# Performance work log

Measured on AMD Instinct MI355X. Metric: run time of the kernel, lower is better.

## Reference

```python
import jax, jax.numpy as jnp
import numpy as np

B, D, C = 4, 49, 512          # batch, tokens, in_features
N = 27                        # main nodes
NSUB = 14                     # sub nodes
C2 = C // 2                   # cross-attn q/k dim
BN_EPS = 1e-5
SCALE = C2 ** -0.5
# sub_list = [0,1,2,4,7,8,11]; each main node feeds two sub-sc rows
SUB_IDX = np.repeat(np.array([0, 1, 2, 4, 7, 8, 11]), 2)  # length 14


def _bn(x, w, b, axes):
    # training-mode batch norm (biased variance), matching nn.BatchNorm* forward math
    m = x.mean(axis=axes, keepdims=True)
    v = x.var(axis=axes, keepdims=True)
    return (x - m) * jax.lax.rsqrt(v + BN_EPS) * w + b


def _l2n(v):
    return v / jnp.maximum(jnp.linalg.norm(v, axis=-1, keepdims=True), 1e-12)


def setup_inputs() -> dict:
    key = jax.random.key(0)
    ks = iter(jax.random.split(key, 40))
    sC = float(np.sqrt(2.0 / C))
    sC2 = float(np.sqrt(2.0 / C2))
    W = lambda k, shape, sc: jax.random.normal(k, shape, jnp.float32) * sc
    inp = {}
    inp['x'] = jax.random.normal(next(ks), (B, D, C), jnp.float32)
    # 27 per-node LinearBlocks (fc + BN1d + relu), stacked
    inp['nb_W'] = W(next(ks), (N, C, C), sC)
    inp['nb_b'] = jnp.zeros((N, C), jnp.float32)
    inp['nb_bnw'] = jnp.ones((N, C), jnp.float32)
    inp['nb_bnb'] = jnp.zeros((N, C), jnp.float32)
    # FAM / ARM cross-attention params (torch Linear: [out,in] + bias)
    inp['fam_qW'] = W(next(ks), (C2, C), sC2); inp['fam_qb'] = jnp.zeros((C2,), jnp.float32)
    inp['fam_kW'] = W(next(ks), (C2, C), sC2); inp['fam_kb'] = jnp.zeros((C2,), jnp.float32)
    inp['fam_vW'] = W(next(ks), (C, C), sC);   inp['fam_vb'] = jnp.zeros((C,), jnp.float32)
    inp['arm_qW'] = W(next(ks), (C2, C), sC2); inp['arm_qb'] = jnp.zeros((C2,), jnp.float32)
    inp['arm_kW'] = W(next(ks), (C2, C), sC2); inp['arm_kb'] = jnp.zeros((C2,), jnp.float32)
    inp['arm_vW'] = W(next(ks), (C, C), sC);   inp['arm_vb'] = jnp.zeros((C,), jnp.float32)
    inp['ep_W'] = W(next(ks), (C, C), sC)
    inp['ep_b'] = jnp.zeros((C,), jnp.float32)
    inp['gem_bnw'] = jnp.ones((N * N,), jnp.float32)
    inp['gem_bnb'] = jnp.zeros((N * N,), jnp.float32)
    # 2 GatedGNN layers, 5 bias-free linears each
    inp['gnn_uW'] = W(next(ks), (2, C, C), sC)
    inp['gnn_vW'] = W(next(ks), (2, C, C), sC)
    inp['gnn_aW'] = W(next(ks), (2, C, C), sC)
    inp['gnn_bW'] = W(next(ks), (2, C, C), sC)
    inp['gnn_eW'] = W(next(ks), (2, C, C), sC)
    inp['gnn_bnvw'] = jnp.ones((2, N), jnp.float32)
    inp['gnn_bnvb'] = jnp.zeros((2, N), jnp.float32)
    inp['gnn_bnew'] = jnp.ones((2, N * N), jnp.float32)
    inp['gnn_bneb'] = jnp.zeros((2, N * N), jnp.float32)
    # similarity-calculation anchors (xavier-ish)
    inp['main_sc'] = W(next(ks), (N, C), float(np.sqrt(2.0 / (N + C))))
    inp['sub_sc'] = W(next(ks), (NSUB, C), float(np.sqrt(2.0 / (NSUB + C))))
    return inp


def _forward(x, nb_W, nb_b, nb_bnw, nb_bnb,
             fam_qW, fam_qb, fam_kW, fam_kb, fam_vW, fam_vb,
             arm_qW, arm_qb, arm_kW, arm_kb, arm_vW, arm_vb,
             ep_W, ep_b, gem_bnw, gem_bnb,
             gnn_uW, gnn_vW, gnn_aW, gnn_bW, gnn_eW,
             gnn_bnvw, gnn_bnvb, gnn_bnew, gnn_bneb,
             main_sc, sub_sc):
    # --- per-main-node LinearBlock, vmapped over the N node layers ---
    def node_block(W, b, bw, bb):
        h = x @ W.T + b                                   # [B,D,C]
        return jax.nn.relu(_bn(h, bw, bb, (0, 1)))        # BN1d over (batch, tokens)
    f_u = jax.vmap(node_block, in_axes=0, out_axes=1)(nb_W, nb_b, nb_bnw, nb_bnb)  # [B,N,D,C]
    f_v = f_u.mean(axis=2)                                # GAP -> [B,N,C]

    # --- GraphEdgeModel: FAM cross-attention (node tokens attend to global tokens) ---
    q = jnp.einsum('bndc,hc->bndh', f_u, fam_qW) + fam_qb # [B,N,D,C2]
    k = x @ fam_kW.T + fam_kb                             # [B,D,C2] (global feature = x, broadcast over N)
    v = x @ fam_vW.T + fam_vb                             # [B,D,C]
    attn = jax.nn.softmax(jnp.einsum('bndh,beh->bnde', q, k) * SCALE, axis=-1)
    feat = jnp.einsum('bnde,bec->bndc', attn, v)          # [B,N,D,C]

    # --- ARM cross-attention over all node pairs: edge e=i*N+j, query=feat[j] (start), key/value=feat[i] (end) ---
    Q = jnp.einsum('bndc,hc->bndh', feat, arm_qW) + arm_qb
    K = jnp.einsum('bndc,hc->bndh', feat, arm_kW) + arm_kb
    V = jnp.einsum('bndc,hc->bndh', feat, arm_vW) + arm_vb  # [B,N,D,C]
    dots = jnp.einsum('bjdh,bieh->bijde', Q, K) * SCALE     # [B,N,N,D,D]
    a2 = jax.nn.softmax(dots, axis=-1)
    fe = jnp.einsum('bijde,biec->bijdc', a2, V).reshape(B, N * N, D, C)

    edge = _bn(fe @ ep_W.T + ep_b,
               gem_bnw.reshape(1, -1, 1, 1), gem_bnb.reshape(1, -1, 1, 1), (0, 2, 3))
    f_e = edge.mean(axis=2).reshape(B, N, N, C)           # GAP over tokens -> [B,N,N,C]

    # --- 2 GatedGNN layers; start/end indicator einsums realized as broadcasts ---
    for l in range(2):
        res = f_v
        vi = f_v @ gnn_aW[l].T                            # end node i contribution
        vj = f_v @ gnn_bW[l].T                            # start node j contribution
        el = f_e @ gnn_eW[l].T
        m = vi[:, :, None, :] + vj[:, None, :, :] + el    # [B,N,N,C]
        m = _bn(m, gnn_bnew[l].reshape(1, N, N, 1), gnn_bneb[l].reshape(1, N, N, 1), (0, 3))
        f_e = f_e + jax.nn.relu(m)
        e = jax.nn.softmax(jax.nn.sigmoid(f_e), axis=2)   # softmax over start nodes j
        uj = f_v @ gnn_vW[l].T
        ui = f_v @ gnn_uW[l].T
        agg = ui + jnp.einsum('bijc,bjc->bic', e, uj) / N # scatter back to end node i
        f_v = res + jax.nn.relu(_bn(agg, gnn_bnvw[l].reshape(1, N, 1), gnn_bnvb[l].reshape(1, N, 1), (0, 2)))

    # --- SC layer: cosine similarity against relu+normalized anchors ---
    fvn = _l2n(f_v)
    main_cl = jnp.einsum('bnc,nc->bn', fvn, _l2n(jax.nn.relu(main_sc)))   # [B,27]
    sub_cl = jnp.einsum('bkc,kc->bk', fvn[:, SUB_IDX], _l2n(jax.nn.relu(sub_sc)))  # [B,14]
    return jnp.concatenate([main_cl, sub_cl], axis=-1)    # [B,41]


def reference(x, nb_W, nb_b, nb_bnw, nb_bnb,
              fam_qW, fam_qb, fam_kW, fam_kb, fam_vW, fam_vb,
              arm_qW, arm_qb, arm_kW, arm_kb, arm_vW, arm_vb,
              ep_W, ep_b, gem_bnw, gem_bnb,
              gnn_uW, gnn_vW, gnn_aW, gnn_bW, gnn_eW,
              gnn_bnvw, gnn_bnvb, gnn_bnew, gnn_bneb,
              main_sc, sub_sc):
    return _forward(x, nb_W, nb_b, nb_bnw, nb_bnb,
                    fam_qW, fam_qb, fam_kW, fam_kb, fam_vW, fam_vb,
                    arm_qW, arm_qb, arm_kW, arm_kb, arm_vW, arm_vb,
                    ep_W, ep_b, gem_bnw, gem_bnb,
                    gnn_uW, gnn_vW, gnn_aW, gnn_bW, gnn_eW,
                    gnn_bnvw, gnn_bnvb, gnn_bnew, gnn_bneb,
                    main_sc, sub_sc)
```

## Files before the change

kernel.cpp:

```cpp
#include <hip/hip_runtime.h>
#include <hip/hip_bf16.h>
#include <math.h>


namespace {

constexpr float SCALE_ = 0.0625f;
constexpr float EPS_   = 1e-5f;

typedef __attribute__((ext_vector_type(8))) short bf16x8;
typedef __attribute__((ext_vector_type(4))) short s16x4;
typedef __attribute__((ext_vector_type(4))) float f32x4;

__device__ __forceinline__ short f2bf(float f) {
  unsigned u = __float_as_uint(f);
  u += 0x7fffu + ((u >> 16) & 1u);
  return (short)(u >> 16);
}
__device__ __forceinline__ float bf2f(short h) {
  return __uint_as_float(((unsigned)(unsigned short)h) << 16);
}
__device__ __forceinline__ void split2(float f, short& h, short& l) {
  h = f2bf(f);
  l = f2bf(f - bf2f(h));
}

template<int CONVB>
__device__ __forceinline__
void gemm_bf3_core(const short* __restrict__ Ah, const short* __restrict__ Al,
                   const short* __restrict__ Wh, const short* __restrict__ Wl,
                   const float* __restrict__ Wf,
                   const float* __restrict__ bias, float* __restrict__ C,
                   short* __restrict__ Ch, short* __restrict__ Cl,
                   int M, int N, int K)
{
  __shared__ short sA[2][64][40];
  __shared__ short sB[2][64][40];
  const int tid  = threadIdx.x;
  const int n0   = blockIdx.x * 64, m0 = blockIdx.y * 64;
  const int wave = tid >> 6, lane = tid & 63;
  const int wr = (wave >> 1) * 32, wc = (wave & 1) * 32;
  const int lr = lane & 15, lk = (lane >> 4) * 8;
  const int sr = tid >> 2, sk = (tid & 3) * 8;
  const int arow = m0 + sr;

  f32x4 acc[2][2] = {};

  for (int k0 = 0; k0 < K; k0 += 32) {
    bf16x8 ah = {}, al = {};
    if (arow < M) {
      ah = *(const bf16x8*)(Ah + (long)arow * K + k0 + sk);
      al = *(const bf16x8*)(Al + (long)arow * K + k0 + sk);
    }
    bf16x8 bh, bl;
    if (CONVB) {
      f32x4 w0 = *(const f32x4*)(Wf + (long)(n0 + sr) * K + k0 + sk);
      f32x4 w1 = *(const f32x4*)(Wf + (long)(n0 + sr) * K + k0 + sk + 4);
#pragma unroll
      for (int j = 0; j < 4; ++j) {
        short h, l;
        split2(w0[j], h, l); bh[j] = h;     bl[j] = l;
        split2(w1[j], h, l); bh[4 + j] = h; bl[4 + j] = l;
      }
    } else {
      bh = *(const bf16x8*)(Wh + (long)(n0 + sr) * K + k0 + sk);
      bl = *(const bf16x8*)(Wl + (long)(n0 + sr) * K + k0 + sk);
    }
    __syncthreads();
    *(bf16x8*)&sA[0][sr][sk] = ah;
    *(bf16x8*)&sA[1][sr][sk] = al;
    *(bf16x8*)&sB[0][sr][sk] = bh;
    *(bf16x8*)&sB[1][sr][sk] = bl;
    __syncthreads();

    bf16x8 a0h = *(const bf16x8*)&sA[0][wr + lr][lk];
    bf16x8 a1h = *(const bf16x8*)&sA[0][wr + 16 + lr][lk];
    bf16x8 a0l = *(const bf16x8*)&sA[1][wr + lr][lk];
    bf16x8 a1l = *(const bf16x8*)&sA[1][wr + 16 + lr][lk];
    bf16x8 b0h = *(const bf16x8*)&sB[0][wc + lr][lk];
    bf16x8 b1h = *(const bf16x8*)&sB[0][wc + 16 + lr][lk];
    bf16x8 b0l = *(const bf16x8*)&sB[1][wc + lr][lk];
    bf16x8 b1l = *(const bf16x8*)&sB[1][wc + 16 + lr][lk];

    acc[0][0] = __builtin_amdgcn_mfma_f32_16x16x32_bf16(a0h, b0h, acc[0][0], 0, 0, 0);
    acc[0][1] = __builtin_amdgcn_mfma_f32_16x16x32_bf16(a0h, b1h, acc[0][1], 0, 0, 0);
    acc[1][0] = __builtin_amdgcn_mfma_f32_16x16x32_bf16(a1h, b0h, acc[1][0], 0, 0, 0);
    acc[1][1] = __builtin_amdgcn_mfma_f32_16x16x32_bf16(a1h, b1h, acc[1][1], 0, 0, 0);
    acc[0][0] = __builtin_amdgcn_mfma_f32_16x16x32_bf16(a0h, b0l, acc[0][0], 0, 0, 0);
    acc[0][1] = __builtin_amdgcn_mfma_f32_16x16x32_bf16(a0h, b1l, acc[0][1], 0, 0, 0);
    acc[1][0] = __builtin_amdgcn_mfma_f32_16x16x32_bf16(a1h, b0l, acc[1][0], 0, 0, 0);
    acc[1][1] = __builtin_amdgcn_mfma_f32_16x16x32_bf16(a1h, b1l, acc[1][1], 0, 0, 0);
    acc[0][0] = __builtin_amdgcn_mfma_f32_16x16x32_bf16(a0l, b0h, acc[0][0], 0, 0, 0);
    acc[0][1] = __builtin_amdgcn_mfma_f32_16x16x32_bf16(a0l, b1h, acc[0][1], 0, 0, 0);
    acc[1][0] = __builtin_amdgcn_mfma_f32_16x16x32_bf16(a1l, b0h, acc[1][0], 0, 0, 0);
    acc[1][1] = __builtin_amdgcn_mfma_f32_16x16x32_bf16(a1l, b1h, acc[1][1], 0, 0, 0);
  }

  const int rbase = m0 + wr + (lane >> 4) * 4;
  const int cb = n0 + wc + lr;
#pragma unroll
  for (int fj = 0; fj < 2; ++fj) {
    int col = cb + fj * 16;
    float bz = bias ? bias[col] : 0.f;
#pragma unroll
    for (int fi = 0; fi < 2; ++fi) {
#pragma unroll
      for (int r = 0; r < 4; ++r) {
        int row = rbase + fi * 16 + r;
        if (row < M) {
          float v = acc[fi][fj][r] + bz;
          long o = (long)row * N + col;
          if (C) C[o] = v;
          if (Ch) { short h, l; split2(v, h, l); Ch[o] = h; Cl[o] = l; }
        }
      }
    }
  }
}

template<int CONVB>
__global__ __launch_bounds__(256)
void gemm_bf3_k(const short* Ah, const short* Al, const short* Wh, const short* Wl,
                const float* Wf, const float* bias, float* C, short* Ch, short* Cl,
                int M, int N, int K, long aBS, long wBS, long bBS, long cBS)
{
  long z = blockIdx.z;
  gemm_bf3_core<CONVB>(Ah + z * aBS, Al + z * aBS,
                       Wh ? Wh + z * wBS : nullptr, Wl ? Wl + z * wBS : nullptr,
                       Wf ? Wf + z * wBS : nullptr,
                       bias ? bias + z * bBS : nullptr,
                       C ? C + z * cBS : nullptr,
                       Ch ? Ch + z * cBS : nullptr, Cl ? Cl + z * cBS : nullptr,
                       M, N, K);
}

struct G4 { const short* wh[4]; const short* wl[4]; float* c[4]; };

__global__ __launch_bounds__(256)
void gemm4_bf3_k(const short* Ah, const short* Al, G4 g, int M, int N, int K)
{
  int z = blockIdx.z;
  gemm_bf3_core<0>(Ah, Al, g.wh[z], g.wl[z], nullptr, nullptr, g.c[z],
                   nullptr, nullptr, M, N, K);
}

__global__ __launch_bounds__(256)
void cvt1_k(const float* __restrict__ s, short* __restrict__ dh,
            short* __restrict__ dl, int n4)
{
  long i = (long)blockIdx.x * 256 + threadIdx.x;
  if (i >= n4) return;
  f32x4 v = *(const f32x4*)(s + i * 4);
  s16x4 h, l;
#pragma unroll
  for (int j = 0; j < 4; ++j) { short hh, ll; split2(v[j], hh, ll); h[j] = hh; l[j] = ll; }
  *(s16x4*)(dh + i * 4) = h;
  *(s16x4*)(dl + i * 4) = l;
}

struct P10 { const float* s[10]; };

__global__ __launch_bounds__(256)
void cvt_w_k(P10 p, short* __restrict__ dh, short* __restrict__ dl)
{
  static const int tens[26] = {0,1,2,3,4,4,5,5,5,5,6,6,6,6,7,7,7,7,8,8,8,8,9,9,9,9};
  static const int coff[26] = {0,0,0,0,0,1,0,1,2,3,0,1,2,3,0,1,2,3,0,1,2,3,0,1,2,3};
  int c = blockIdx.y;
  const float* src = p.s[tens[c]] + (long)coff[c] * 131072;
  long dbase = (long)c * 131072;
  long i = ((long)blockIdx.x * 256 + threadIdx.x) * 8;
  f32x4 v0 = *(const f32x4*)(src + i);
  f32x4 v1 = *(const f32x4*)(src + i + 4);
  s16x4 h0, l0, h1, l1;
#pragma unroll
  for (int j = 0; j < 4; ++j) {
    short hh, ll;
    split2(v0[j], hh, ll); h0[j] = hh; l0[j] = ll;
    split2(v1[j], hh, ll); h1[j] = hh; l1[j] = ll;
  }
  *(s16x4*)(dh + dbase + i) = h0;     *(s16x4*)(dh + dbase + i + 4) = h1;
  *(s16x4*)(dl + dbase + i) = l0;     *(s16x4*)(dl + dbase + i + 4) = l1;
}

__global__ __launch_bounds__(256)
void gemm_nn_k(const float* __restrict__ A, const float* __restrict__ W,
               float* __restrict__ C, int M, int N, int K)
{
  __shared__ float As[32][68];
  __shared__ float Ws[32][68];
  const int tid = threadIdx.x;
  const int n0 = blockIdx.x * 64, m0 = blockIdx.y * 64;
  const int tx = tid & 15, ty = tid >> 4;
  float acc[4][4] = {};
  for (int k0 = 0; k0 < K; k0 += 32) {
#pragma unroll
    for (int p = 0; p < 2; ++p) {
      int idx = tid + p * 256;
      int row = idx >> 3, kq = idx & 7;
      float4 v = make_float4(0.f, 0.f, 0.f, 0.f);
      if (m0 + row < M)
        v = *(const float4*)(A + (long)(m0 + row) * K + k0 + kq * 4);
      As[kq*4+0][row] = v.x; As[kq*4+1][row] = v.y;
      As[kq*4+2][row] = v.z; As[kq*4+3][row] = v.w;
    }
#pragma unroll
    for (int p = 0; p < 2; ++p) {
      int idx = tid + p * 256;
      int row = idx >> 4, nq = idx & 15;
      float4 v = *(const float4*)(W + (long)(k0 + row) * N + n0 + nq * 4);
      *(float4*)&Ws[row][nq*4] = v;
    }
    __syncthreads();
#pragma unroll
    for (int k = 0; k < 32; ++k) {
      float4 a4 = *(const float4*)&As[k][ty*4];
      float4 b4 = *(const float4*)&Ws[k][tx*4];
      float av[4] = {a4.x, a4.y, a4.z, a4.w};
      float bv[4] = {b4.x, b4.y, b4.z, b4.w};
#pragma unroll
      for (int i2 = 0; i2 < 4; ++i2)
#pragma unroll
        for (int j2 = 0; j2 < 4; ++j2)
          acc[i2][j2] = fmaf(av[i2], bv[j2], acc[i2][j2]);
    }
    __syncthreads();
  }
#pragma unroll
  for (int i2 = 0; i2 < 4; ++i2) {
    int m = m0 + ty*4 + i2;
    if (m < M)
      *(float4*)(C + (long)m * N + n0 + tx*4) =
        make_float4(acc[i2][0], acc[i2][1], acc[i2][2], acc[i2][3]);
  }
}

__global__ __launch_bounds__(256)
void nb_stats(const float* __restrict__ H, float* __restrict__ mean, float* __restrict__ rs)
{
  int n = blockIdx.x;
  int c = blockIdx.y * 256 + threadIdx.x;
  const float* p = H + (long)n * 196 * 512 + c;
  float s = 0.f, q = 0.f;
  for (int r = 0; r < 196; ++r) { float v = p[(long)r * 512]; s += v; q = fmaf(v, v, q); }
  float m = s * (1.f / 196.f);
  float var = q * (1.f / 196.f) - m * m;
  mean[n * 512 + c] = m;
  rs[n * 512 + c] = rsqrtf(var + EPS_);
}

__global__ __launch_bounds__(256)
void nb_apply(const float* __restrict__ H, const float* __restrict__ mean,
              const float* __restrict__ rs, const float* __restrict__ bw,
              const float* __restrict__ bb,
              short* __restrict__ fuh, short* __restrict__ ful,
              float* __restrict__ fv, short* __restrict__ fvh, short* __restrict__ fvl)
{
  int n = blockIdx.x, b = blockIdx.y;
  int t = threadIdx.x;
#pragma unroll
  for (int cq = 0; cq < 2; ++cq) {
    int c = cq * 256 + t;
    float m = mean[n*512+c], r = rs[n*512+c];
    float w = bw[n*512+c], bias = bb[n*512+c];
    const float* hp = H + ((long)(n*4+b)*49) * 512 + c;
    long fo0 = ((long)(n*4+b)*49) * 512 + c;
    float s = 0.f;
    for (int d = 0; d < 49; ++d) {
      float v = hp[(long)d*512];
      float o = fmaxf(fmaf((v - m) * r, w, bias), 0.f);
      short hh, ll; split2(o, hh, ll);
      fuh[fo0 + (long)d*512] = hh;
      ful[fo0 + (long)d*512] = ll;
      s += o;
    }
    float fvv = s * (1.f / 49.f);
    long fo = ((long)b*27+n)*512 + c;
    fv[fo] = fvv;
    short hh, ll; split2(fvv, hh, ll);
    fvh[fo] = hh; fvl[fo] = ll;
  }
}

__global__ __launch_bounds__(512)
void attn_fam(const float* __restrict__ Qg, const float* __restrict__ Kg,
              const float* __restrict__ Vg, short* __restrict__ feath,
              short* __restrict__ featl)
{
  __shared__ float Qs[52][68];
  __shared__ float Ks[52][68];
  __shared__ float Ss[49][56];
  __shared__ float Vs[49][68];

  const int tid = threadIdx.x;
  const int bx = blockIdx.x, b = blockIdx.y;
  const int qblk = bx*4 + b;
  const long obase = ((long)b*1323 + (long)bx*49) * 512;
  const float* qp = Qg + (long)qblk * (49 * 256);
  const float* kp = Kg + (long)b * (49 * 256);
  const float* vp = Vg + (long)b * (49 * 512);

  const int tx = tid & 15;
  const int ty4 = tid >> 4;

  float sacc[2][4] = {};
  const int d0 = ty4 * 2;
  const int e0 = tx * 4;
  const int eh0 = (e0+0)&7, eh1 = (e0+1)&7, eh2 = (e0+2)&7, eh3 = (e0+3)&7;
  const int er0 = (e0+0) > 51 ? 51 : (e0+0);
  const int er1 = (e0+1) > 51 ? 51 : (e0+1);
  const int er2 = (e0+2) > 51 ? 51 : (e0+2);
  const int er3 = (e0+3) > 51 ? 51 : (e0+3);
  for (int kc = 0; kc < 256; kc += 64) {
    for (int idx = tid; idx < 49 * 16; idx += 512) {
      int row = idx >> 4, kq = idx & 15;
      *(float4*)&Qs[row][kq*4] = *(const float4*)(qp + (long)row*256 + kc + kq*4);
      *(float4*)&Ks[row][(kq ^ (row & 7)) * 4] = *(const float4*)(kp + (long)row*256 + kc + kq*4);
    }
    __syncthreads();
    if (d0 < 49) {
      const float* q0 = &Qs[d0][0];
      const float* q1 = &Qs[d0 + 1][0];
      const float* k0 = &Ks[er0][0];
      const float* k1 = &Ks[er1][0];
      const float* k2 = &Ks[er2][0];
      const float* k3 = &Ks[er3][0];
#pragma unroll 4
      for (int kq = 0; kq < 16; ++kq) {
        float4 a0 = *(const float4*)(q0 + kq*4);
        float4 a1 = *(const float4*)(q1 + kq*4);
        float4 b0 = *(const float4*)(k0 + ((kq ^ eh0) * 4));
        float4 b1 = *(const float4*)(k1 + ((kq ^ eh1) * 4));
        float4 b2 = *(const float4*)(k2 + ((kq ^ eh2) * 4));
        float4 b3 = *(const float4*)(k3 + ((kq ^ eh3) * 4));
        float av0[4] = {a0.x, a0.y, a0.z, a0.w};
        float av1[4] = {a1.x, a1.y, a1.z, a1.w};
        float bv[4][4] = {{b0.x,b0.y,b0.z,b0.w},{b1.x,b1.y,b1.z,b1.w},
                          {b2.x,b2.y,b2.z,b2.w},{b3.x,b3.y,b3.z,b3.w}};
#pragma unroll
        for (int j2 = 0; j2 < 4; ++j2) {
#pragma unroll
          for (int qq = 0; qq < 4; ++qq) {
            sacc[0][j2] = fmaf(av0[qq], bv[j2][qq], sacc[0][j2]);
            sacc[1][j2] = fmaf(av1[qq], bv[j2][qq], sacc[1][j2]);
          }
        }
      }
    }
    __syncthreads();
  }
  if (d0 < 49) {
#pragma unroll
    for (int i2 = 0; i2 < 2; ++i2) {
      int d = d0 + i2;
      if (d < 49) {
#pragma unroll
        for (int j2 = 0; j2 < 4; ++j2) {
          int e = e0 + j2;
          if (e < 49) Ss[d][e] = sacc[i2][j2] * SCALE_;
        }
      }
    }
  }
  __syncthreads();

  if (tid < 49) {
    float mx = -1e30f;
    for (int e = 0; e < 49; ++e) mx = fmaxf(mx, Ss[tid][e]);
    float sum = 0.f;
    for (int e = 0; e < 49; ++e) { float ex = __expf(Ss[tid][e] - mx); Ss[tid][e] = ex; sum += ex; }
    float inv = 1.f / sum;
    for (int e = 0; e < 49; ++e) Ss[tid][e] *= inv;
  }
  __syncthreads();

  const int td = ty4;
  const bool has2 = (td + 32) < 49;
  for (int cc = 0; cc < 512; cc += 64) {
    for (int idx = tid; idx < 49 * 16; idx += 512) {
      int row = idx >> 4, cq = idx & 15;
      *(float4*)&Vs[row][cq*4] = *(const float4*)(vp + (long)row*512 + cc + cq*4);
    }
    __syncthreads();
    float pa[2][4] = {};
#pragma unroll 7
    for (int e = 0; e < 49; ++e) {
      float4 v4 = *(const float4*)&Vs[e][tx*4];
      float p0 = Ss[td][e];
      float p1 = has2 ? Ss[td + 32][e] : 0.f;
      pa[0][0] = fmaf(p0, v4.x, pa[0][0]); pa[0][1] = fmaf(p0, v4.y, pa[0][1]);
      pa[0][2] = fmaf(p0, v4.z, pa[0][2]); pa[0][3] = fmaf(p0, v4.w, pa[0][3]);
      pa[1][0] = fmaf(p1, v4.x, pa[1][0]); pa[1][1] = fmaf(p1, v4.y, pa[1][1]);
      pa[1][2] = fmaf(p1, v4.z, pa[1][2]); pa[1][3] = fmaf(p1, v4.w, pa[1][3]);
    }
    __syncthreads();
    s16x4 hh, ll;
#pragma unroll
    for (int j = 0; j < 4; ++j) { short h, l; split2(pa[0][j], h, l); hh[j] = h; ll[j] = l; }
    *(s16x4*)(feath + obase + (long)td*512 + cc + tx*4) = hh;
    *(s16x4*)(featl + obase + (long)td*512 + cc + tx*4) = ll;
    if (has2) {
#pragma unroll
      for (int j = 0; j < 4; ++j) { short h, l; split2(pa[1][j], h, l); hh[j] = h; ll[j] = l; }
      *(s16x4*)(feath + obase + (long)(td+32)*512 + cc + tx*4) = hh;
      *(s16x4*)(featl + obase + (long)(td+32)*512 + cc + tx*4) = ll;
    }
  }
}

__global__ __launch_bounds__(512)
void bias2red_k(const float* __restrict__ epW, const float* __restrict__ vb,
                const float* __restrict__ epb, float* __restrict__ bias2,
                float* __restrict__ b2st)
{
  int c = threadIdx.x;
  float s = epb[c];
  const float* r = epW + (long)c * 512;
  for (int k = 0; k < 512; ++k) s = fmaf(r[k], vb[k], s);
  bias2[c] = s;
  __shared__ float red[16];
  float s1 = s, s2 = s * s;
#pragma unroll
  for (int off = 32; off; off >>= 1) { s1 += __shfl_down(s1, off); s2 += __shfl_down(s2, off); }
  int lane = c & 63, wid = c >> 6;
  if (lane == 0) { red[wid] = s1; red[8 + wid] = s2; }
  __syncthreads();
  if (c == 0) {
    float a = 0.f, qq = 0.f;
#pragma unroll
    for (int w = 0; w < 8; ++w) { a += red[w]; qq += red[8 + w]; }
    b2st[0] = a; b2st[1] = qq;
  }
}

__constant__ unsigned char TI_c[28] = {0,1,1,2,2,2,3,3,3,3,4,4,4,4,4,5,5,5,5,5,5,6,6,6,6,6,6,6};
__constant__ unsigned char TJ_c[28] = {0,0,1,0,1,2,0,1,2,3,0,1,2,3,4,0,1,2,3,4,5,0,1,2,3,4,5,6};

__global__ __launch_bounds__(256)
void gmat_k(const float* __restrict__ VW, const float* __restrict__ b2,
            float* __restrict__ G, float* __restrict__ V1, float* __restrict__ Vb2)
{
  __shared__ float Vs[49][260];
  const int i = blockIdx.x, b = blockIdx.y;
  const int tid = threadIdx.x;
  const int wave = tid >> 6, lane = tid & 63;
  const int di = lane >> 3, ej = lane & 7;
  const float* vp = VW + ((long)b*1323 + (long)i*49) * 512;
  float gacc[7];
#pragma unroll
  for (int t = 0; t < 7; ++t) gacc[t] = 0.f;
  float s1 = 0.f, s2 = 0.f;

  for (int half = 0; half < 2; ++half) {
    __syncthreads();
    for (int idx = tid; idx < 49 * 64; idx += 256) {
      int r = idx >> 6, q = idx & 63;
      *(float4*)&Vs[r][q*4] = *(const float4*)(vp + (long)r*512 + half*256 + q*4);
    }
    __syncthreads();
    int tt = 0;
    for (int t = wave; t < 28; t += 4, ++tt) {
      int d = TI_c[t]*8 + di, e = TJ_c[t]*8 + ej;
      int dc = d > 48 ? 48 : d, ec = e > 48 ? 48 : e;
      float g = gacc[tt];
      for (int q = 0; q < 64; ++q) {
        float4 a = *(const float4*)&Vs[dc][q*4];
        float4 bq = *(const float4*)&Vs[ec][q*4];
        g = fmaf(a.x, bq.x, fmaf(a.y, bq.y, fmaf(a.z, bq.z, fmaf(a.w, bq.w, g))));
      }
      gacc[tt] = g;
    }
    if (tid < 49) {
      for (int c = 0; c < 256; ++c) {
        float v = Vs[tid][c];
        s1 += v; s2 = fmaf(v, b2[half*256 + c], s2);
      }
    }
  }
  long gbase = ((long)b*27 + i) * 2401;
  int tt = 0;
  for (int t = wave; t < 28; t += 4, ++tt) {
    int ti = TI_c[t], tj = TJ_c[t];
    int d = ti*8 + di, e = tj*8 + ej;
    if (d < 49 && e < 49) {
      G[gbase + d*49 + e] = gacc[tt];
      if (ti != tj) G[gbase + e*49 + d] = gacc[tt];
    }
  }
  if (tid < 49) {
    long o = ((long)b*27 + i) * 49 + tid;
    V1[o] = s1; Vb2[o] = s2;
  }
}

__global__ __launch_bounds__(64)
void arm_post(const float* __restrict__ S, const float* __restrict__ G,
              const float* __restrict__ V1, const float* __restrict__ Vb2,
              float* __restrict__ Pbar, float* __restrict__ parts)
{
  __shared__ float TP[49 * 53];
  __shared__ float TG[49 * 53];
  const int tid = threadIdx.x;
  const int x = blockIdx.x, b = blockIdx.y;
  const int i = x / 27, j = x - i * 27;
  const float* Sp = S + (long)b*1323*1344 + (long)j*49*1344 + (long)i*49;
  for (int idx = tid; idx < 2401; idx += 64) {
    unsigned d = ((unsigned)idx * 1338u) >> 16;
    unsigned e = (unsigned)idx - d * 49u;
    TP[d*53 + e] = Sp[(long)d*1344 + e];
  }
  const float* Gp = G + ((long)b*27 + i) * 2401;
  for (int idx = tid; idx < 2401; idx += 64) {
    unsigned d = ((unsigned)idx * 1338u) >> 16;
    unsigned e = (unsigned)idx - d * 49u;
    TG[d*53 + e] = Gp[idx];
  }
  __syncthreads();
  if (tid < 49) {
    float* pr = &TP[tid * 53];
    float mx = -1e30f;
    for (int e = 0; e < 49; ++e) mx = fmaxf(mx, pr[e]);
    float sum = 0.f;
    for (int e = 0; e < 49; ++e) { float ex = __expf(pr[e] - mx); pr[e] = ex; sum += ex; }
    float inv = 1.f / sum;
    for (int e = 0; e < 49; ++e) pr[e] *= inv;
  }
  __syncthreads();
  float lin = 0.f, pvb = 0.f;
  if (tid < 49) {
    float pb = 0.f;
    for (int d = 0; d < 49; ++d) pb += TP[d*53 + tid];
    Pbar[(((long)b*27 + i)*27 + j)*49 + tid] = pb;
    long vo = ((long)b*27 + i)*49 + tid;
    lin = pb * V1[vo];
    pvb = pb * Vb2[vo];
  }
  float q2 = 0.f;
  if (tid < 49) {
    const float* pr = &TP[tid * 53];
#pragma unroll 1
    for (int e = 0; e < 49; e += 7) {
      float t0=0.f,t1=0.f,t2=0.f,t3=0.f,t4=0.f,t5=0.f,t6=0.f;
      for (int e2 = 0; e2 < 49; ++e2) {
        float pv = pr[e2];
        const float* g = &TG[e2*53 + e];
        t0 = fmaf(pv, g[0], t0); t1 = fmaf(pv, g[1], t1);
        t2 = fmaf(pv, g[2], t2); t3 = fmaf(pv, g[3], t3);
        t4 = fmaf(pv, g[4], t4); t5 = fmaf(pv, g[5], t5);
        t6 = fmaf(pv, g[6], t6);
      }
      q2 += t0*pr[e] + t1*pr[e+1] + t2*pr[e+2] + t3*pr[e+3]
          + t4*pr[e+4] + t5*pr[e+5] + t6*pr[e+6];
    }
  }
  float r1 = lin, r2 = q2 + 2.f * pvb;
#pragma unroll
  for (int off = 32; off; off >>= 1) { r1 += __shfl_down(r1, off); r2 += __shfl_down(r2, off); }
  if (tid == 0) {
    long o = ((long)b*729 + x) * 2;
    parts[o] = r1; parts[o + 1] = r2;
  }
}

__global__ __launch_bounds__(256)
void edge_fin(const float* __restrict__ parts, const float* __restrict__ b2st,
              float* __restrict__ ems)
{
  int e = blockIdx.x * 256 + threadIdx.x;
  if (e < 729) {
    float B1 = b2st[0], nb2 = b2st[1];
    float s = 196.f * B1, q = 196.f * nb2;
#pragma unroll
    for (int b = 0; b < 4; ++b) {
      s += parts[((long)b * 729 + e) * 2 + 0];
      q += parts[((long)b * 729 + e) * 2 + 1];
    }
    const float inv = 1.f / 100352.f;
    float m = s * inv;
    float var = q * inv - m * m;
    ems[e*2]   = m;
    ems[e*2+1] = rsqrtf(var + EPS_);
  }
}

__global__ __launch_bounds__(256)
void fe_build(const float* __restrict__ Pbar, const float* __restrict__ VW,
              const float* __restrict__ b2, const float* __restrict__ ems,
              const float* __restrict__ gw, const float* __restrict__ gb,
              float* __restrict__ fe, short* __restrict__ feh, short* __restrict__ fel)
{
  __shared__ float Pb[27 * 49];
  const int i = blockIdx.x, b = blockIdx.y;
  const int tid = threadIdx.x;
  const float* pp = Pbar + ((long)b*27 + i) * 27 * 49;
  for (int idx = tid; idx < 1323; idx += 256) Pb[idx] = pp[idx];
  __syncthreads();
  const float* vp = VW + ((long)b*1323 + (long)i*49) * 512;
#pragma unroll 1
  for (int half = 0; half < 2; ++half) {
    int c = half * 256 + tid;
    float acc[27];
#pragma unroll
    for (int j = 0; j < 27; ++j) acc[j] = 0.f;
    for (int e = 0; e < 49; ++e) {
      float v = vp[(long)e*512 + c];
#pragma unroll
      for (int j = 0; j < 27; ++j) acc[j] = fmaf(Pb[j*49 + e], v, acc[j]);
    }
    float bz = b2[c];
#pragma unroll
    for (int j = 0; j < 27; ++j) {
      int ij = i*27 + j;
      float m = ems[ij*2], rs = ems[ij*2+1];
      float h = acc[j] * (1.f/49.f) + bz;
      float v = fmaf((h - m) * rs, gw[ij], gb[ij]);
      long o = ((long)b*729 + ij)*512 + c;
      fe[o] = v;
      short hh, ll; split2(v, hh, ll);
      feh[o] = hh; fel[o] = ll;
    }
  }
}

__global__ __launch_bounds__(256)
void gnn_edge_bn(const float* __restrict__ vi, const float* __restrict__ vj,
                 const float* __restrict__ el, const float* __restrict__ wv,
                 const float* __restrict__ bv, float* fe,
                 short* __restrict__ feh, short* __restrict__ fel)
{
  int ij = blockIdx.x; int i = ij / 27, j = ij - i * 27;
  int t = threadIdx.x;
  __shared__ float red[18];
  float mv[8]; float s = 0.f, q = 0.f;
#pragma unroll
  for (int p = 0; p < 8; ++p) {
    int idx = p * 256 + t; int b = idx >> 9, c = idx & 511;
    float v = vi[((long)b*27+i)*512 + c] + vj[((long)b*27+j)*512 + c]
            + el[((long)b*729+ij)*512 + c];
    mv[p] = v; s += v; q = fmaf(v, v, q);
  }
  int lane = t & 63, wid = t >> 6;
#pragma unroll
  for (int off = 32; off; off >>= 1) { s += __shfl_down(s, off); q += __shfl_down(q, off); }
  if (lane == 0) { red[wid] = s; red[4 + wid] = q; }
  __syncthreads();
  if (t == 0) {
    float S = red[0]+red[1]+red[2]+red[3], Q = red[4]+red[5]+red[6]+red[7];
    float m = S * (1.f / 2048.f);
    red[16] = m;
    red[17] = rsqrtf(Q * (1.f / 2048.f) - m * m + EPS_);
  }
  __syncthreads();
  float m = red[16], rs = red[17];
  float w = wv[ij], bb = bv[ij];
#pragma unroll
  for (int p = 0; p < 8; ++p) {
    int idx = p * 256 + t; int b = idx >> 9, c = idx & 511;
    long o = ((long)b*729+ij)*512 + c;
    float nv = fe[o] + fmaxf(fmaf((mv[p] - m) * rs, w, bb), 0.f);
    fe[o] = nv;
    short hh, ll; split2(nv, hh, ll);
    feh[o] = hh; fel[o] = ll;
  }
}

__global__ __launch_bounds__(256)
void gnn_agg(const float* __restrict__ fe, const float* __restrict__ ui,
             const float* __restrict__ uj, float* __restrict__ agg)
{
  int i = blockIdx.x, b = blockIdx.y;
  int t = threadIdx.x;
#pragma unroll
  for (int cq = 0; cq < 2; ++cq) {
    int c = cq * 256 + t;
    float sg[27];
    float mx = -1e30f;
#pragma unroll
    for (int j = 0; j < 27; ++j) {
      float x = fe[((long)b*729 + i*27 + j)*512 + c];
      float sgm = 1.f / (1.f + __expf(-x));
      sg[j] = sgm; mx = fmaxf(mx, sgm);
    }
    float sum = 0.f;
#pragma unroll
    for (int j = 0; j < 27; ++j) { float e2 = __expf(sg[j] - mx); sg[j] = e2; sum += e2; }
    float acc = 0.f;
#pragma unroll
    for (int j = 0; j < 27; ++j)
      acc = fmaf(sg[j], uj[((long)b*27+j)*512 + c], acc);
    agg[((long)b*27+i)*512 + c] = ui[((long)b*27+i)*512 + c] + acc / (sum * 27.f);
  }
}

__global__ __launch_bounds__(256)
void gnn_node_bn(const float* __restrict__ agg, const float* __restrict__ wv,
                 const float* __restrict__ bv, float* fv,
                 short* __restrict__ fvh, short* __restrict__ fvl)
{
  int i = blockIdx.x;
  int t = threadIdx.x;
  __shared__ float red[18];
  float mv[8]; float s = 0.f, q = 0.f;
#pragma unroll
  for (int p = 0; p < 8; ++p) {
    int idx = p * 256 + t; int b = idx >> 9, c = idx & 511;
    float v = agg[((long)b*27+i)*512 + c];
    mv[p] = v; s += v; q = fmaf(v, v, q);
  }
  int lane = t & 63, wid = t >> 6;
#pragma unroll
  for (int off = 32; off; off >>= 1) { s += __shfl_down(s, off); q += __shfl_down(q, off); }
  if (lane == 0) { red[wid] = s; red[4 + wid] = q; }
  __syncthreads();
  if (t == 0) {
    float S = red[0]+red[1]+red[2]+red[3], Q = red[4]+red[5]+red[6]+red[7];
    float m = S * (1.f / 2048.f);
    red[16] = m;
    red[17] = rsqrtf(Q * (1.f / 2048.f) - m * m + EPS_);
  }
  __syncthreads();
  float m = red[16], rs = red[17];
  float w = wv[i], bb = bv[i];
#pragma unroll
  for (int p = 0; p < 8; ++p) {
    int idx = p * 256 + t; int b = idx >> 9, c = idx & 511;
    long o = ((long)b*27+i)*512 + c;
    float nv = fv[o] + fmaxf(fmaf((mv[p] - m) * rs, w, bb), 0.f);
    fv[o] = nv;
    short hh, ll; split2(nv, hh, ll);
    fvh[o] = hh; fvl[o] = ll;
  }
}

__constant__ int SUB_IDX_c[14] = {0,0,1,1,2,2,4,4,7,7,8,8,11,11};

__global__ __launch_bounds__(64)
void sc_k(const float* __restrict__ fv, const float* __restrict__ mainsc,
          const float* __restrict__ subsc, float* __restrict__ out)
{
  int o = blockIdx.x, b = blockIdx.y;
  int lane = threadIdx.x;
  int r; const float* ap;
  if (o < 27) { r = o; ap = mainsc + (long)o * 512; }
  else        { int k = o - 27; r = SUB_IDX_c[k]; ap = subsc + (long)k * 512; }
  const float* fp = fv + ((long)b*27 + r) * 512;
  float sff = 0.f, saa = 0.f, sfa = 0.f;
  for (int c = lane; c < 512; c += 64) {
    float f = fp[c];
    float a = fmaxf(ap[c], 0.f);
    sff = fmaf(f, f, sff); saa = fmaf(a, a, saa); sfa = fmaf(f, a, sfa);
  }
#pragma unroll
  for (int off = 32; off; off >>= 1) {
    sff += __shfl_down(sff, off); saa += __shfl_down(saa, off); sfa += __shfl_down(sfa, off);
  }
  if (lane == 0)
    out[b * 41 + o] = sfa / (fmaxf(sqrtf(sff), 1e-12f) * fmaxf(sqrtf(saa), 1e-12f));
}

}

extern "C" void kernel_launch(void* const* d_in, const int* in_sizes, int n_in,
                              void* d_out, int out_size, void* d_ws, size_t ws_size,
                              hipStream_t stream)
{
  (void)in_sizes; (void)n_in; (void)out_size; (void)ws_size;
  const float* x       = (const float*)d_in[0];
  const float* nb_W    = (const float*)d_in[1];
  const float* nb_b    = (const float*)d_in[2];
  const float* nb_bnw  = (const float*)d_in[3];
  const float* nb_bnb  = (const float*)d_in[4];
  const float* fam_qW  = (const float*)d_in[5];
  const float* fam_qb  = (const float*)d_in[6];
  const float* fam_kW  = (const float*)d_in[7];
  const float* fam_kb  = (const float*)d_in[8];
  const float* fam_vW  = (const float*)d_in[9];
  const float* fam_vb  = (const float*)d_in[10];
  const float* arm_qW  = (const float*)d_in[11];
  const float* arm_qb  = (const float*)d_in[12];
  const float* arm_kW  = (const float*)d_in[13];
  const float* arm_kb  = (const float*)d_in[14];
  const float* arm_vW  = (const float*)d_in[15];
  const float* arm_vb  = (const float*)d_in[16];
  const float* ep_W    = (const float*)d_in[17];
  const float* ep_b    = (const float*)d_in[18];
  const float* gem_bnw = (const float*)d_in[19];
  const float* gem_bnb = (const float*)d_in[20];
  const float* gnn_uW  = (const float*)d_in[21];
  const float* gnn_vW  = (const float*)d_in[22];
  const float* gnn_aW  = (const float*)d_in[23];
  const float* gnn_bW  = (const float*)d_in[24];
  const float* gnn_eW  = (const float*)d_in[25];
  const float* gnn_bnvw = (const float*)d_in[26];
  const float* gnn_bnvb = (const float*)d_in[27];
  const float* gnn_bnew = (const float*)d_in[28];
  const float* gnn_bneb = (const float*)d_in[29];
  const float* main_sc  = (const float*)d_in[30];
  const float* sub_sc   = (const float*)d_in[31];
  float* out = (float*)d_out;

  char* wp = (char*)d_ws;
  auto carveF = [&](long n) -> float* { float* p = (float*)wp; wp += ((n + 15) & ~15L) * 4; return p; };
  auto carveS = [&](long n) -> short* { short* p = (short*)wp; wp += ((n + 15) & ~15L) * 2; return p; };

  float* Hnb   = carveF((long)27*196*512);
  float* S     = carveF((long)4*1323*1344);
  float* fe    = carveF((long)4*729*512);
  float* kf    = carveF(196*256);
  float* vf    = carveF(196*512);
  float* qfam  = carveF((long)5292*256);
  float* nbm   = carveF(27*512);
  float* nbr   = carveF(27*512);
  float* Mpre  = carveF(512*512);
  float* bias2 = carveF(512);
  float* b2st  = carveF(16);
  float* parts = carveF(4*729*2);
  float* ems   = carveF(1460);
  float* G     = carveF((long)108*2401);
  float* V1    = carveF(108*49);
  float* Vb2   = carveF(108*49);
  float* Pbar  = carveF((long)4*27*27*49);
  float* fv    = carveF(108*512);
  float* vi    = carveF(108*512);
  float* vj    = carveF(108*512);
  float* uj    = carveF(108*512);
  float* ui    = carveF(108*512);
  float* agg   = carveF(108*512);
  float* VW = Hnb;
  float* el = S;

  short* xh    = carveS(100352);
  short* xl    = carveS(100352);
  short* wph   = carveS((long)26*131072);
  short* wpl   = carveS((long)26*131072);
  short* Mpreh = carveS(262144);
  short* Mprel = carveS(262144);
  short* fuh   = carveS((long)5292*512);
  short* ful   = carveS((long)5292*512);
  short* Qah   = carveS((long)5292*256);
  short* Qal   = carveS((long)5292*256);
  short* Kah   = carveS((long)4*1344*256);
  short* Kal   = carveS((long)4*1344*256);
  short* fvh   = carveS(108*512);
  short* fvl   = carveS(108*512);
  short* feath = fuh;
  short* featl = ful;
  short* feh   = Qah;
  short* fel   = Qal;
  fel = Kah;

  short* famqWh = wph + 0L*131072;        short* famqWl = wpl + 0L*131072;
  short* famkWh = wph + 1L*131072;        short* famkWl = wpl + 1L*131072;
  short* armqWh = wph + 2L*131072;        short* armqWl = wpl + 2L*131072;
  short* armkWh = wph + 3L*131072;        short* armkWl = wpl + 3L*131072;
  short* famvWh = wph + 4L*131072;        short* famvWl = wpl + 4L*131072;
  short* uWh    = wph + 6L*131072;        short* uWl    = wpl + 6L*131072;
  short* vWh    = wph + 10L*131072;       short* vWl    = wpl + 10L*131072;
  short* aWh    = wph + 14L*131072;       short* aWl    = wpl + 14L*131072;
  short* bWh    = wph + 18L*131072;       short* bWl    = wpl + 18L*131072;
  short* eWh    = wph + 22L*131072;       short* eWl    = wpl + 22L*131072;

  cvt1_k<<<dim3(98), 256, 0, stream>>>(x, xh, xl, 25088);
  P10 p10;
  p10.s[0] = fam_qW; p10.s[1] = fam_kW; p10.s[2] = arm_qW; p10.s[3] = arm_kW;
  p10.s[4] = fam_vW; p10.s[5] = gnn_uW; p10.s[6] = gnn_vW; p10.s[7] = gnn_aW;
  p10.s[8] = gnn_bW; p10.s[9] = gnn_eW;
  cvt_w_k<<<dim3(64, 26), 256, 0, stream>>>(p10, wph, wpl);

  gemm_bf3_k<1><<<dim3(8,4,27), 256, 0, stream>>>(xh, xl, nullptr, nullptr, nb_W,
      nb_b, Hnb, nullptr, nullptr, 196, 512, 512, 0, 262144, 512, 100352);
  nb_stats<<<dim3(27,2), 256, 0, stream>>>(Hnb, nbm, nbr);
  nb_apply<<<dim3(27,4), 256, 0, stream>>>(Hnb, nbm, nbr, nb_bnw, nb_bnb,
      fuh, ful, fv, fvh, fvl);
  gemm_bf3_k<0><<<dim3(4,4), 256, 0, stream>>>(xh, xl, famkWh, famkWl, nullptr,
      fam_kb, kf, nullptr, nullptr, 196, 256, 512, 0,0,0,0);
  gemm_bf3_k<0><<<dim3(8,4), 256, 0, stream>>>(xh, xl, famvWh, famvWl, nullptr,
      fam_vb, vf, nullptr, nullptr, 196, 512, 512, 0,0,0,0);
  gemm_bf3_k<0><<<dim3(4,83), 256, 0, stream>>>(fuh, ful, famqWh, famqWl, nullptr,
      fam_qb, qfam, nullptr, nullptr, 5292, 256, 512, 0,0,0,0);
  attn_fam<<<dim3(27,4), 512, 0, stream>>>(qfam, kf, vf, feath, featl);
  gemm_bf3_k<0><<<dim3(4,83), 256, 0, stream>>>(feath, featl, armqWh, armqWl, nullptr,
      arm_qb, nullptr, Qah, Qal, 5292, 256, 512, 0,0,0,0);
  gemm_bf3_k<0><<<dim3(4,21,4), 256, 0, stream>>>(feath, featl, armkWh, armkWl, nullptr,
      arm_kb, nullptr, Kah, Kal, 1323, 256, 512, (long)1323*512, 0, 0, (long)1344*256);
  gemm_nn_k<<<dim3(8,8), 256, 0, stream>>>(ep_W, arm_vW, Mpre, 512, 512, 512);
  cvt1_k<<<dim3(256), 256, 0, stream>>>(Mpre, Mpreh, Mprel, 65536);
  bias2red_k<<<dim3(1), 512, 0, stream>>>(ep_W, arm_vb, ep_b, bias2, b2st);
  gemm_bf3_k<0><<<dim3(8,83), 256, 0, stream>>>(feath, featl, Mpreh, Mprel, nullptr,
      nullptr, VW, nullptr, nullptr, 5292, 512, 512, 0,0,0,0);
  gemm_bf3_k<0><<<dim3(21,21,4), 256, 0, stream>>>(Qah, Qal, Kah, Kal, nullptr,
      nullptr, S, nullptr, nullptr, 1323, 1344, 256,
      (long)1323*256, (long)1344*256, 0, (long)1323*1344);
  gmat_k<<<dim3(27,4), 256, 0, stream>>>(VW, bias2, G, V1, Vb2);
  arm_post<<<dim3(729,4), 64, 0, stream>>>(S, G, V1, Vb2, Pbar, parts);
  edge_fin<<<dim3(3), 256, 0, stream>>>(parts, b2st, ems);
  fe_build<<<dim3(27,4), 256, 0, stream>>>(Pbar, VW, bias2, ems, gem_bnw, gem_bnb,
      fe, feh, fel);
  for (int l = 0; l < 2; ++l) {
    long wo = (long)l * 262144;
    G4 g4;
    g4.wh[0] = aWh + wo; g4.wl[0] = aWl + wo; g4.c[0] = vi;
    g4.wh[1] = bWh + wo; g4.wl[1] = bWl + wo; g4.c[1] = vj;
    g4.wh[2] = vWh + wo; g4.wl[2] = vWl + wo; g4.c[2] = uj;
    g4.wh[3] = uWh + wo; g4.wl[3] = uWl + wo; g4.c[3] = ui;
    gemm4_bf3_k<<<dim3(8,2,4), 256, 0, stream>>>(fvh, fvl, g4, 108, 512, 512);
    gemm_bf3_k<0><<<dim3(8,46), 256, 0, stream>>>(feh, fel, eWh + wo, eWl + wo, nullptr,
        nullptr, el, nullptr, nullptr, 2916, 512, 512, 0,0,0,0);
    gnn_edge_bn<<<dim3(729), 256, 0, stream>>>(vi, vj, el,
        gnn_bnew + (long)l*729, gnn_bneb + (long)l*729, fe, feh, fel);
    gnn_agg<<<dim3(27,4), 256, 0, stream>>>(fe, ui, uj, agg);
    gnn_node_bn<<<dim3(27), 256, 0, stream>>>(agg,
        gnn_bnvw + (long)l*27, gnn_bnvb + (long)l*27, fv, fvh, fvl);
  }
  sc_k<<<dim3(41,4), 64, 0, stream>>>(fv, main_sc, sub_sc, out);
}
```

Before: 685.8 us.

## Restructure arm_post quadratic form via P^T P Gram and widen to 128 threads

```diff
diff --git a/kernel.cpp b/kernel.cpp
--- a/kernel.cpp
+++ b/kernel.cpp
@@ -492,31 +492,30 @@
   }
 }
 
-__global__ __launch_bounds__(64)
+__global__ __launch_bounds__(128)
 void arm_post(const float* __restrict__ S, const float* __restrict__ G,
               const float* __restrict__ V1, const float* __restrict__ Vb2,
               float* __restrict__ Pbar, float* __restrict__ parts)
 {
-  __shared__ float TP[49 * 53];
-  __shared__ float TG[49 * 53];
+  __shared__ float TP[49 * 56];
+  __shared__ float red[8];
   const int tid = threadIdx.x;
   const int x = blockIdx.x, b = blockIdx.y;
   const int i = x / 27, j = x - i * 27;
   const float* Sp = S + (long)b*1323*1344 + (long)j*49*1344 + (long)i*49;
-  for (int idx = tid; idx < 2401; idx += 64) {
+  for (int idx = tid; idx < 2401; idx += 128) {
     unsigned d = ((unsigned)idx * 1338u) >> 16;
     unsigned e = (unsigned)idx - d * 49u;
-    TP[d*53 + e] = Sp[(long)d*1344 + e];
-  }
-  const float* Gp = G + ((long)b*27 + i) * 2401;
-  for (int idx = tid; idx < 2401; idx += 64) {
-    unsigned d = ((unsigned)idx * 1338u) >> 16;
-    unsigned e = (unsigned)idx - d * 49u;
-    TG[d*53 + e] = Gp[idx];
-  }
-  __syncthreads();
+    TP[d*56 + e] = Sp[(long)d*1344 + e];
+  }
+  for (int idx = tid; idx < 343; idx += 128) {
+    int d = idx / 7, e = 49 + idx - d * 7;
+    TP[d*56 + e] = 0.f;
+  }
+  __syncthreads();
+
   if (tid < 49) {
-    float* pr = &TP[tid * 53];
+    float* pr = &TP[tid * 56];
     float mx = -1e30f;
     for (int e = 0; e < 49; ++e) mx = fmaxf(mx, pr[e]);
     float sum = 0.f;
@@ -525,39 +524,51 @@
     for (int e = 0; e < 49; ++e) pr[e] *= inv;
   }
   __syncthreads();
+
   float lin = 0.f, pvb = 0.f;
   if (tid < 49) {
     float pb = 0.f;
-    for (int d = 0; d < 49; ++d) pb += TP[d*53 + tid];
+    for (int d = 0; d < 49; ++d) pb += TP[d*56 + tid];
     Pbar[(((long)b*27 + i)*27 + j)*49 + tid] = pb;
     long vo = ((long)b*27 + i)*49 + tid;
     lin = pb * V1[vo];
     pvb = pb * Vb2[vo];
   }
+
   float q2 = 0.f;
-  if (tid < 49) {
-    const float* pr = &TP[tid * 53];
-#pragma unroll 1
-    for (int e = 0; e < 49; e += 7) {
-      float t0=0.f,t1=0.f,t2=0.f,t3=0.f,t4=0.f,t5=0.f,t6=0.f;
-      for (int e2 = 0; e2 < 49; ++e2) {
-        float pv = pr[e2];
-        const float* g = &TG[e2*53 + e];
-        t0 = fmaf(pv, g[0], t0); t1 = fmaf(pv, g[1], t1);
-        t2 = fmaf(pv, g[2], t2); t3 = fmaf(pv, g[3], t3);
-        t4 = fmaf(pv, g[4], t4); t5 = fmaf(pv, g[5], t5);
-        t6 = fmaf(pv, g[6], t6);
-      }
-      q2 += t0*pr[e] + t1*pr[e+1] + t2*pr[e+2] + t3*pr[e+3]
-          + t4*pr[e+4] + t5*pr[e+5] + t6*pr[e+6];
-    }
-  }
+  const float* Gp = G + ((long)b*27 + i) * 2401;
+  for (int s = tid; s < 343; s += 128) {
+    int e = s / 7;
+    int k8 = (s - e * 7) * 8;
+    float t[8];
+#pragma unroll
+    for (int k = 0; k < 8; ++k) t[k] = 0.f;
+    for (int d = 0; d < 49; ++d) {
+      float pe = TP[d*56 + e];
+      f32x4 a = *(const f32x4*)&TP[d*56 + k8];
+      f32x4 bq = *(const f32x4*)&TP[d*56 + k8 + 4];
+      t[0] = fmaf(pe, a[0], t[0]); t[1] = fmaf(pe, a[1], t[1]);
+      t[2] = fmaf(pe, a[2], t[2]); t[3] = fmaf(pe, a[3], t[3]);
+      t[4] = fmaf(pe, bq[0], t[4]); t[5] = fmaf(pe, bq[1], t[5]);
+      t[6] = fmaf(pe, bq[2], t[6]); t[7] = fmaf(pe, bq[3], t[7]);
+    }
+    const float* g = Gp + e * 49 + k8;
+    int lim = 49 - k8;
+#pragma unroll
+    for (int k = 0; k < 8; ++k)
+      if (k < lim) q2 = fmaf(t[k], g[k], q2);
+  }
+
   float r1 = lin, r2 = q2 + 2.f * pvb;
 #pragma unroll
   for (int off = 32; off; off >>= 1) { r1 += __shfl_down(r1, off); r2 += __shfl_down(r2, off); }
+  int lane = tid & 63, wid = tid >> 6;
+  if (lane == 0) { red[wid] = r1; red[2 + wid] = r2; }
+  __syncthreads();
   if (tid == 0) {
     long o = ((long)b*729 + x) * 2;
-    parts[o] = r1; parts[o + 1] = r2;
+    parts[o]     = red[0] + red[1];
+    parts[o + 1] = red[2] + red[3];
   }
 }
 
@@ -845,8 +856,7 @@
   short* feath = fuh;
   short* featl = ful;
   short* feh   = Qah;
-  short* fel   = Qal;
-  fel = Kah;
+  short* fel   = Kah;
 
   short* famqWh = wph + 0L*131072;        short* famqWl = wpl + 0L*131072;
   short* famkWh = wph + 1L*131072;        short* famkWl = wpl + 1L*131072;
@@ -891,7 +901,7 @@
       nullptr, S, nullptr, nullptr, 1323, 1344, 256,
       (long)1323*256, (long)1344*256, 0, (long)1323*1344);
   gmat_k<<<dim3(27,4), 256, 0, stream>>>(VW, bias2, G, V1, Vb2);
-  arm_post<<<dim3(729,4), 64, 0, stream>>>(S, G, V1, Vb2, Pbar, parts);
+  arm_post<<<dim3(729,4), 128, 0, stream>>>(S, G, V1, Vb2, Pbar, parts);
   edge_fin<<<dim3(3), 256, 0, stream>>>(parts, b2st, ems);
   fe_build<<<dim3(27,4), 256, 0, stream>>>(Pbar, VW, bias2, ems, gem_bnw, gem_bnb,
       fe, feh, fel);
```

After: 685.5 us. No clear change (-0.0%).
